# Performance work log

Hardware: AMD Instinct MI355X
Metric: run time of the kernel (lower is better)

The kernel has to match this reference:

```python
import jax, jax.numpy as jnp
import numpy as np

DIM = 1024
N_HEADS = 16
HEAD_DIM = DIM // N_HEADS


def setup_inputs() -> dict:
    key = jax.random.key(0)
    k_x, k_qkv_w, k_qkv_b, k_p_w, k_p_b = jax.random.split(key, 5)
    s = 1.0 / np.sqrt(DIM)
    return {
        "x": jax.random.normal(k_x, (2, 2048, DIM), dtype=jnp.float32),
        # stored as [in, out] so forward is x @ W + b (equivalent to torch Linear)
        "qkv_w": jax.random.uniform(k_qkv_w, (DIM, 3 * DIM), minval=-s, maxval=s, dtype=jnp.float32),
        "qkv_b": jax.random.uniform(k_qkv_b, (3 * DIM,), minval=-s, maxval=s, dtype=jnp.float32),
        "proj_w": jax.random.uniform(k_p_w, (DIM, DIM), minval=-s, maxval=s, dtype=jnp.float32),
        "proj_b": jax.random.uniform(k_p_b, (DIM,), minval=-s, maxval=s, dtype=jnp.float32),
    }


def reference(x, qkv_w, qkv_b, proj_w, proj_b):
    b, s, _ = x.shape
    qkv = x @ qkv_w + qkv_b                       # [b, s, 3*dim]
    q, k, v = jnp.split(qkv, 3, axis=-1)
    def split_heads(t):
        return t.reshape(b, s, N_HEADS, HEAD_DIM).transpose(0, 2, 1, 3)  # [b, h, s, d]
    q, k, v = map(split_heads, (q, k, v))
    scale = 1.0 / np.sqrt(HEAD_DIM)
    scores = jnp.einsum("bhqd,bhkd->bhqk", q, k) * scale
    attn = jax.nn.softmax(scores, axis=-1)
    out = jnp.einsum("bhqk,bhkd->bhqd", attn, v)
    out = out.transpose(0, 2, 1, 3).reshape(b, s, DIM)
    return out @ proj_w + proj_b
```

## Files before the change

### kernel.cpp

```cpp
#include <hip/hip_runtime.h>
#include <hip/hip_bf16.h>

typedef __attribute__((ext_vector_type(8))) short bf16x8;
typedef __attribute__((ext_vector_type(4))) float f32x4;
typedef __attribute__((ext_vector_type(16))) float f32x16;
typedef __attribute__((ext_vector_type(4))) unsigned short u16x4;
typedef __attribute__((ext_vector_type(8))) unsigned short u16x8v;

#define S_LEN 2048
#define NHEAD 16
#define HDIM 64
#define DIM 1024

__device__ __forceinline__ unsigned short f2bf(float f) {
    union { float f; unsigned u; } x; x.f = f;
    unsigned r = x.u + 0x7FFFu + ((x.u >> 16) & 1u);
    return (unsigned short)(r >> 16);
}
__device__ __forceinline__ unsigned short f2bf_fast(float f) {
    union { float f; unsigned u; } x; x.f = f;
    return (unsigned short)((x.u + 0x8000u) >> 16);
}

__device__ __forceinline__ f32x4 mfma16(bf16x8 a, bf16x8 b, f32x4 c) {
    return __builtin_amdgcn_mfma_f32_16x16x32_bf16(a, b, c, 0, 0, 0);
}
__device__ __forceinline__ f32x16 mfma32(bf16x8 a, bf16x8 b, f32x16 c) {
    return __builtin_amdgcn_mfma_f32_32x32x16_bf16(a, b, c, 0, 0, 0);
}

__device__ __forceinline__ float fexp2(float x) {
#if __has_builtin(__builtin_amdgcn_exp2f)
    return __builtin_amdgcn_exp2f(x);
#else
    return exp2f(x);
#endif
}

__device__ __forceinline__ void gl_lds16(const void* g, void* l) {
    __builtin_amdgcn_global_load_lds(
        (const __attribute__((address_space(1))) unsigned int*)g,
        (__attribute__((address_space(3))) unsigned int*)l, 16, 0, 0);
}

__global__ __launch_bounds__(256) void xconv_kernel(const float* __restrict__ X,
                                                    unsigned short* __restrict__ Xb) {
    size_t i = ((size_t)blockIdx.x * 256 + threadIdx.x) * 8;
    float4 a = *reinterpret_cast<const float4*>(&X[i]);
    float4 b = *reinterpret_cast<const float4*>(&X[i + 4]);
    u16x8v o;
    o[0] = f2bf(a.x); o[1] = f2bf(a.y); o[2] = f2bf(a.z); o[3] = f2bf(a.w);
    o[4] = f2bf(b.x); o[5] = f2bf(b.y); o[6] = f2bf(b.z); o[7] = f2bf(b.w);
    *reinterpret_cast<u16x8v*>(&Xb[i]) = o;
}

__global__ __launch_bounds__(256) void wtrans_kernel(const float* __restrict__ W,
                                                     unsigned short* __restrict__ Wt,
                                                     int K, int N) {
    __shared__ float lds[64][65];
    int k0 = blockIdx.x * 64, n0 = blockIdx.y * 64;
    int tid = threadIdx.x;
    for (int idx = tid; idx < 1024; idx += 256) {
        int row = idx >> 4, c = (idx & 15) << 2;
        float4 v = *reinterpret_cast<const float4*>(&W[(size_t)(k0 + row) * N + n0 + c]);
        lds[row][c] = v.x; lds[row][c + 1] = v.y; lds[row][c + 2] = v.z; lds[row][c + 3] = v.w;
    }
    __syncthreads();
    for (int idx = tid; idx < 1024; idx += 256) {
        int row = idx >> 4, c = (idx & 15) << 2;
        u16x4 o;
        o[0] = f2bf(lds[c][row]);     o[1] = f2bf(lds[c + 1][row]);
        o[2] = f2bf(lds[c + 2][row]); o[3] = f2bf(lds[c + 3][row]);
        *reinterpret_cast<u16x4*>(&Wt[(size_t)(n0 + row) * K + k0 + c]) = o;
    }
}

template <int MODE>
__global__ __launch_bounds__(256) void gemm_kernel(
    const unsigned short* __restrict__ Ab, const unsigned short* __restrict__ Bt,
    const float* __restrict__ bias,
    unsigned short* __restrict__ Qb, unsigned short* __restrict__ Kb,
    unsigned short* __restrict__ Vt, float* __restrict__ outf) {
    __shared__ unsigned short Alds[128 * 64];
    __shared__ unsigned short Blds[128 * 64];
    const int tid = threadIdx.x;
    const int m0 = blockIdx.x * 128, n0 = blockIdx.y * 128;
    const int wid = tid >> 6, lane = tid & 63;
    const int wm = wid >> 1, wn = wid & 1;
    const int lr = lane & 15, lg = lane >> 4;

    const char* Abase = (const char*)(Ab + (size_t)m0 * 1024);
    const char* Bbase = (const char*)(Bt + (size_t)n0 * 1024);

    int srcOff[4], dstOff[4];
#pragma unroll
    for (int i = 0; i < 4; ++i) {
        int off = i * 4096 + wid * 1024 + lane * 16;
        int row = off >> 7, col = off & 127;
        srcOff[i] = row * 2048 + (col ^ ((row & 7) << 4));
        dstOff[i] = off;
    }
    const int swz = (lr & 7) << 4;

    f32x4 acc[4][4] = {};

    for (int kt = 0; kt < 16; ++kt) {
        __syncthreads();
#pragma unroll
        for (int i = 0; i < 4; ++i) {
            gl_lds16(Abase + srcOff[i] + kt * 128, (char*)Alds + dstOff[i]);
            gl_lds16(Bbase + srcOff[i] + kt * 128, (char*)Blds + dstOff[i]);
        }
        __syncthreads();

#pragma unroll
        for (int ks = 0; ks < 2; ++ks) {
            bf16x8 af[4], bfr[4];
#pragma unroll
            for (int i = 0; i < 4; ++i)
                af[i] = *reinterpret_cast<const bf16x8*>(
                    (const char*)Alds + (wm * 64 + i * 16 + lr) * 128 + ((ks * 64 + lg * 16) ^ swz));
#pragma unroll
            for (int j = 0; j < 4; ++j)
                bfr[j] = *reinterpret_cast<const bf16x8*>(
                    (const char*)Blds + (wn * 64 + j * 16 + lr) * 128 + ((ks * 64 + lg * 16) ^ swz));
            __builtin_amdgcn_s_setprio(1);
#pragma unroll
            for (int i = 0; i < 4; ++i)
#pragma unroll
                for (int j = 0; j < 4; ++j)
                    acc[i][j] = mfma16(af[i], bfr[j], acc[i][j]);
            __builtin_amdgcn_s_setprio(0);
        }
    }

    if constexpr (MODE == 0) {
        const int sec = n0 >> 10;
#pragma unroll
        for (int j = 0; j < 4; ++j) {
            int gn = n0 + wn * 64 + j * 16 + lr;
            float bv = bias[gn];
            int nn = gn & 1023, h = nn >> 6, d = nn & 63;
#pragma unroll
            for (int i = 0; i < 4; ++i) {
#pragma unroll
                for (int r = 0; r < 4; ++r) {
                    int m = m0 + wm * 64 + i * 16 + lg * 4 + r;
                    int b_ = m >> 11, s_ = m & 2047;
                    size_t bh = (size_t)(b_ * NHEAD + h);
                    float v = acc[i][j][r] + bv;
                    if (sec == 0)
                        Qb[(bh * S_LEN + s_) * HDIM + d] = f2bf(v * 0.18033688f);
                    else if (sec == 1)
                        Kb[(bh * S_LEN + s_) * HDIM + d] = f2bf(v);
                    else
                        Vt[(bh * HDIM + d) * S_LEN + s_] = f2bf(v);
                }
            }
        }
    } else {
#pragma unroll
        for (int j = 0; j < 4; ++j) {
            int gn = n0 + wn * 64 + j * 16 + lr;
            float bv = bias[gn];
#pragma unroll
            for (int i = 0; i < 4; ++i) {
#pragma unroll
                for (int r = 0; r < 4; ++r) {
                    int m = m0 + wm * 64 + i * 16 + lg * 4 + r;
                    outf[(size_t)m * DIM + gn] = acc[i][j][r] + bv;
                }
            }
        }
    }
}

__device__ __forceinline__ void repack32(const f32x16& p, bf16x8 (&pa)[2]) {
#pragma unroll
    for (int k2 = 0; k2 < 2; ++k2) {
        const int rb = 8 * k2;
        unsigned aw[2], bw[2];
#pragma unroll
        for (int u = 0; u < 2; ++u) {
            unsigned a, b;
            asm("v_cvt_pk_bf16_f32 %0, %1, %2"
                : "=v"(a) : "v"(p[rb + 2 * u]), "v"(p[rb + 2 * u + 1]));
            asm("v_cvt_pk_bf16_f32 %0, %1, %2"
                : "=v"(b) : "v"(p[rb + 4 + 2 * u]), "v"(p[rb + 4 + 2 * u + 1]));
            asm volatile("v_permlane32_swap_b32 %0, %1" : "+v"(a), "+v"(b));
            aw[u] = a; bw[u] = b;
        }
        union { unsigned w[4]; bf16x8 v; } pu;
        pu.w[0] = aw[0]; pu.w[1] = aw[1]; pu.w[2] = bw[0]; pu.w[3] = bw[1];
        pa[k2] = pu.v;
    }
}

#define NPAIR 16
__global__ __launch_bounds__(512, 4) void attn_kernel(const unsigned short* __restrict__ Qb,
                                                      const unsigned short* __restrict__ Kb,
                                                      const unsigned short* __restrict__ Vt,
                                                      unsigned short* __restrict__ Ob) {
    __shared__ char smem[65536];
    const int L = blockIdx.x;
    const int xcd = L & 7, slot = L >> 3;
    const int bh = xcd + 8 * (slot & 3);
    const int qblk = slot >> 2;
    const int wid = threadIdx.x >> 6;
    const int lane = threadIdx.x & 63;
    const int l31 = lane & 31, hi = lane >> 5;
    const int qs = wid & 3, kh = wid >> 2;
    const int q0 = qblk * 128 + qs * 32;

    const unsigned short* qrow = &Qb[((size_t)bh * S_LEN + q0 + l31) * HDIM];
    bf16x8 qf[4];
#pragma unroll
    for (int kst = 0; kst < 4; ++kst)
        qf[kst] = *reinterpret_cast<const bf16x8*>(&qrow[kst * 16 + hi * 8]);

    const char* kT = (const char*)&Kb[(size_t)bh * S_LEN * HDIM];
    const char* vT = (const char*)&Vt[(size_t)bh * HDIM * S_LEN];

    const char* sbase = (wid < 4) ? kT : vT;
    const int pairStride = (wid < 4) ? 16384 : 256;
    int srcOff[4], dstOff[4];
#pragma unroll
    for (int i = 0; i < 4; ++i) {
        int id = 4 * wid + i;
        if (id < 16) {
            int t2 = (id >> 3) & 1, khs = (id >> 2) & 1, kst = id & 3;
            srcOff[i] = t2 * 8192 + (khs * 32 + l31) * 128 + kst * 32 + hi * 16;
        } else {
            int c = id - 16;
            int t2 = (c >> 3) & 1, khs = (c >> 2) & 1, dt = (c >> 1) & 1, k2 = c & 1;
            srcOff[i] = t2 * 128 + (dt * 32 + l31) * 4096 + khs * 64 + k2 * 32 + hi * 16;
        }
        dstOff[i] = id * 1024;
    }

    float ls = 0.f;
    f32x16 acc[2] = {};

#pragma unroll
    for (int i = 0; i < 4; ++i)
        gl_lds16(sbase + srcOff[i], smem + dstOff[i]);
    __syncthreads();

    int cur = 0;
    for (int pt = 0; pt < NPAIR; ++pt) {
        if (pt + 1 < NPAIR) {
#pragma unroll
            for (int i = 0; i < 4; ++i)
                gl_lds16(sbase + (pt + 1) * pairStride + srcOff[i],
                         smem + (cur ^ 1) * 32768 + dstOff[i]);
        }
#pragma unroll
        for (int t2 = 0; t2 < 2; ++t2) {
            const char* kbb = smem + cur * 32768 + (t2 * 8 + kh * 4) * 1024 + lane * 16;
            const char* vbb = smem + cur * 32768 + 16384 + (t2 * 8 + kh * 4) * 1024 + lane * 16;

            f32x16 p = {};
            __builtin_amdgcn_s_setprio(1);
#pragma unroll
            for (int kst = 0; kst < 4; ++kst) {
                bf16x8 kb = *reinterpret_cast<const bf16x8*>(kbb + kst * 1024);
                p = mfma32(kb, qf[kst], p);
            }
            __builtin_amdgcn_s_setprio(0);

#pragma unroll
            for (int r = 0; r < 16; ++r) {
                float e = fexp2(p[r]); p[r] = e; ls += e;
            }
            bf16x8 pa[2];
            repack32(p, pa);

            __builtin_amdgcn_s_setprio(1);
#pragma unroll
            for (int dt = 0; dt < 2; ++dt)
#pragma unroll
                for (int k2 = 0; k2 < 2; ++k2) {
                    bf16x8 vb = *reinterpret_cast<const bf16x8*>(vbb + (dt * 2 + k2) * 1024);
                    acc[dt] = mfma32(pa[k2], vb, acc[dt]);
                }
            __builtin_amdgcn_s_setprio(0);
        }
        __syncthreads();
        cur ^= 1;
    }

    ls += __shfl_xor(ls, 32, 64);

    float* cacc = (float*)smem;
    float* cls  = (float*)(smem + 32768);
    if (kh == 1) {
#pragma unroll
        for (int dt = 0; dt < 2; ++dt)
#pragma unroll
            for (int r = 0; r < 16; ++r)
                cacc[qs * 2048 + dt * 1024 + r * 64 + lane] = acc[dt][r];
        cls[qs * 32 + l31] = ls;
    }
    __syncthreads();
    if (kh == 0) {
        ls += cls[qs * 32 + l31];
#pragma unroll
        for (int dt = 0; dt < 2; ++dt)
#pragma unroll
            for (int r = 0; r < 16; ++r)
                acc[dt][r] += cacc[qs * 2048 + dt * 1024 + r * 64 + lane];

        const int b_ = bh >> 4, h = bh & 15;
        float inv[16];
#pragma unroll
        for (int r = 0; r < 16; ++r) {
            int rq = (r & 3) + 8 * (r >> 2) + 4 * hi;
            inv[r] = 1.f / __shfl(ls, rq, 64);
        }
#pragma unroll
        for (int dt = 0; dt < 2; ++dt)
#pragma unroll
            for (int r = 0; r < 16; ++r) {
                int rq = (r & 3) + 8 * (r >> 2) + 4 * hi;
                int q = q0 + rq;
                Ob[((size_t)(b_ * S_LEN + q)) * DIM + h * HDIM + dt * 32 + l31] =
                    f2bf_fast(acc[dt][r] * inv[r]);
            }
    }
}

extern "C" void kernel_launch(void* const* d_in, const int* in_sizes, int n_in,
                              void* d_out, int out_size, void* d_ws, size_t ws_size,
                              hipStream_t stream) {
    const float* x      = (const float*)d_in[0];
    const float* qkv_w  = (const float*)d_in[1];
    const float* qkv_b  = (const float*)d_in[2];
    const float* proj_w = (const float*)d_in[3];
    const float* proj_b = (const float*)d_in[4];
    float* out = (float*)d_out;

    unsigned short* Wqkvt = (unsigned short*)d_ws;
    unsigned short* Wpt   = Wqkvt + 3072 * 1024;
    unsigned short* Qb    = Wpt + 1024 * 1024;
    unsigned short* Kb    = Qb + 32 * 2048 * 64;
    unsigned short* Vt    = Kb + 32 * 2048 * 64;
    unsigned short* Ob    = Vt + 32 * 2048 * 64;
    unsigned short* Xb    = Ob + 4096 * 1024;

    xconv_kernel<<<2048, 256, 0, stream>>>(x, Xb);
    wtrans_kernel<<<dim3(16, 48), 256, 0, stream>>>(qkv_w, Wqkvt, 1024, 3072);
    wtrans_kernel<<<dim3(16, 16), 256, 0, stream>>>(proj_w, Wpt, 1024, 1024);

    gemm_kernel<0><<<dim3(32, 24), 256, 0, stream>>>(Xb, Wqkvt, qkv_b, Qb, Kb, Vt, nullptr);
    attn_kernel<<<512, 512, 0, stream>>>(Qb, Kb, Vt, Ob);
    gemm_kernel<1><<<dim3(32, 8), 256, 0, stream>>>(Ob, Wpt, proj_b, nullptr, nullptr, nullptr, out);
}
```

Before: 114.5 us.

## Remap GEMM blocks per XCD, vectorize V stores, compute softmax sums via MFMA

```diff
diff --git a/kernel.cpp b/kernel.cpp
--- a/kernel.cpp
+++ b/kernel.cpp
@@ -75,7 +75,7 @@
     }
 }
 
-template <int MODE>
+template <int MODE, int NBX>
 __global__ __launch_bounds__(256) void gemm_kernel(
     const unsigned short* __restrict__ Ab, const unsigned short* __restrict__ Bt,
     const float* __restrict__ bias,
@@ -84,7 +84,10 @@
     __shared__ unsigned short Alds[128 * 64];
     __shared__ unsigned short Blds[128 * 64];
     const int tid = threadIdx.x;
-    const int m0 = blockIdx.x * 128, n0 = blockIdx.y * 128;
+    const int Lb = blockIdx.x;
+    const int xcd8 = Lb & 7, tt = Lb >> 3;
+    const int m0 = (tt & 31) * 128;
+    const int n0 = (xcd8 * NBX + (tt >> 5)) * 128;
     const int wid = tid >> 6, lane = tid & 63;
     const int wm = wid >> 1, wn = wid & 1;
     const int lr = lane & 15, lg = lane >> 4;
@@ -141,20 +144,30 @@
             int gn = n0 + wn * 64 + j * 16 + lr;
             float bv = bias[gn];
             int nn = gn & 1023, h = nn >> 6, d = nn & 63;
-#pragma unroll
-            for (int i = 0; i < 4; ++i) {
-#pragma unroll
-                for (int r = 0; r < 4; ++r) {
-                    int m = m0 + wm * 64 + i * 16 + lg * 4 + r;
-                    int b_ = m >> 11, s_ = m & 2047;
-                    size_t bh = (size_t)(b_ * NHEAD + h);
-                    float v = acc[i][j][r] + bv;
-                    if (sec == 0)
-                        Qb[(bh * S_LEN + s_) * HDIM + d] = f2bf(v * 0.18033688f);
-                    else if (sec == 1)
-                        Kb[(bh * S_LEN + s_) * HDIM + d] = f2bf(v);
-                    else
-                        Vt[(bh * HDIM + d) * S_LEN + s_] = f2bf(v);
+            if (sec == 2) {
+#pragma unroll
+                for (int i = 0; i < 4; ++i) {
+                    int sb = m0 + wm * 64 + i * 16 + lg * 4;
+                    size_t bhv = (size_t)((sb >> 11) * NHEAD + h);
+                    u16x4 pv;
+#pragma unroll
+                    for (int r = 0; r < 4; ++r) pv[r] = f2bf(acc[i][j][r] + bv);
+                    *reinterpret_cast<u16x4*>(&Vt[(bhv * HDIM + d) * S_LEN + (sb & 2047)]) = pv;
+                }
+            } else {
+#pragma unroll
+                for (int i = 0; i < 4; ++i) {
+#pragma unroll
+                    for (int r = 0; r < 4; ++r) {
+                        int m = m0 + wm * 64 + i * 16 + lg * 4 + r;
+                        int b_ = m >> 11, s_ = m & 2047;
+                        size_t bh = (size_t)(b_ * NHEAD + h);
+                        float v = acc[i][j][r] + bv;
+                        if (sec == 0)
+                            Qb[(bh * S_LEN + s_) * HDIM + d] = f2bf(v * 0.18033688f);
+                        else
+                            Kb[(bh * S_LEN + s_) * HDIM + d] = f2bf(v);
+                    }
                 }
             }
         }
@@ -218,6 +231,10 @@
     for (int kst = 0; kst < 4; ++kst)
         qf[kst] = *reinterpret_cast<const bf16x8*>(&qrow[kst * 16 + hi * 8]);
 
+    bf16x8 onesf;
+#pragma unroll
+    for (int j = 0; j < 8; ++j) onesf[j] = (short)0x3F80;
+
     const char* kT = (const char*)&Kb[(size_t)bh * S_LEN * HDIM];
     const char* vT = (const char*)&Vt[(size_t)bh * HDIM * S_LEN];
 
@@ -238,8 +255,8 @@
         dstOff[i] = id * 1024;
     }
 
-    float ls = 0.f;
     f32x16 acc[2] = {};
+    f32x16 sacc = {};
 
 #pragma unroll
     for (int i = 0; i < 4; ++i)
@@ -269,13 +286,13 @@
             __builtin_amdgcn_s_setprio(0);
 
 #pragma unroll
-            for (int r = 0; r < 16; ++r) {
-                float e = fexp2(p[r]); p[r] = e; ls += e;
-            }
+            for (int r = 0; r < 16; ++r) p[r] = fexp2(p[r]);
             bf16x8 pa[2];
             repack32(p, pa);
 
             __builtin_amdgcn_s_setprio(1);
+            sacc = mfma32(pa[0], onesf, sacc);
+            sacc = mfma32(pa[1], onesf, sacc);
 #pragma unroll
             for (int dt = 0; dt < 2; ++dt)
 #pragma unroll
@@ -289,8 +306,6 @@
         cur ^= 1;
     }
 
-    ls += __shfl_xor(ls, 32, 64);
-
     float* cacc = (float*)smem;
     float* cls  = (float*)(smem + 32768);
     if (kh == 1) {
@@ -299,11 +314,16 @@
 #pragma unroll
             for (int r = 0; r < 16; ++r)
                 cacc[qs * 2048 + dt * 1024 + r * 64 + lane] = acc[dt][r];
-        cls[qs * 32 + l31] = ls;
+        if (l31 == 0) {
+#pragma unroll
+            for (int r = 0; r < 16; ++r) {
+                int rq = (r & 3) + 8 * (r >> 2) + 4 * hi;
+                cls[qs * 32 + rq] = sacc[r];
+            }
+        }
     }
     __syncthreads();
     if (kh == 0) {
-        ls += cls[qs * 32 + l31];
 #pragma unroll
         for (int dt = 0; dt < 2; ++dt)
 #pragma unroll
@@ -315,7 +335,7 @@
 #pragma unroll
         for (int r = 0; r < 16; ++r) {
             int rq = (r & 3) + 8 * (r >> 2) + 4 * hi;
-            inv[r] = 1.f / __shfl(ls, rq, 64);
+            inv[r] = 1.f / (sacc[r] + cls[qs * 32 + rq]);
         }
 #pragma unroll
         for (int dt = 0; dt < 2; ++dt)
@@ -351,7 +371,7 @@
     wtrans_kernel<<<dim3(16, 48), 256, 0, stream>>>(qkv_w, Wqkvt, 1024, 3072);
     wtrans_kernel<<<dim3(16, 16), 256, 0, stream>>>(proj_w, Wpt, 1024, 1024);
 
-    gemm_kernel<0><<<dim3(32, 24), 256, 0, stream>>>(Xb, Wqkvt, qkv_b, Qb, Kb, Vt, nullptr);
+    gemm_kernel<0, 3><<<768, 256, 0, stream>>>(Xb, Wqkvt, qkv_b, Qb, Kb, Vt, nullptr);
     attn_kernel<<<512, 512, 0, stream>>>(Qb, Kb, Vt, Ob);
-    gemm_kernel<1><<<dim3(32, 8), 256, 0, stream>>>(Ob, Wpt, proj_b, nullptr, nullptr, nullptr, out);
-}
+    gemm_kernel<1, 1><<<256, 256, 0, stream>>>(Ob, Wpt, proj_b, nullptr, nullptr, nullptr, out);
+}
```

Result: slower. 126.2 us (+10.3%).
